# Optimization experiments

Hardware: AMD Instinct MI355X
Metric: run time of the kernel (lower is better)

Reference implementation:

```python
import jax, jax.numpy as jnp
import numpy as np
import math

B, S, D, H, F, L = 16, 512, 1024, 16, 4096, 4
DK = D // H
NEG = -1e32


def _cosine_pe(max_len, d_model):
    # deterministic sin/cos table (the 0.1*randn init is fully overwritten for even d_model)
    pos = np.arange(max_len, dtype=np.float32)[:, None]
    div = np.exp(np.arange(0, d_model, 2, dtype=np.float32) * (-(math.log(10000.0) / d_model)))
    pe = np.zeros((max_len, d_model), dtype=np.float32)
    pe[:, 0::2] = np.sin(pos * div)
    pe[:, 1::2] = np.cos(pos * div)
    return jnp.asarray(pe)[None]  # [1, max_len, D]


def setup_inputs() -> dict:
    key = jax.random.key(0)
    ks = jax.random.split(key, 16)
    sc_d = 1.0 / math.sqrt(D)
    sc_f = 1.0 / math.sqrt(F)
    return {
        "q_embed_data": jax.random.normal(ks[0], (B, S, D), jnp.float32),
        "qa_embed_data": jax.random.normal(ks[1], (B, S, D), jnp.float32),
        "pe": _cosine_pe(S, D),
        "Wk": jax.random.normal(ks[2], (L, D, D), jnp.float32) * sc_d,
        "bk": jnp.zeros((L, D), jnp.float32),
        "Wv": jax.random.normal(ks[3], (L, D, D), jnp.float32) * sc_d,
        "bv": jnp.zeros((L, D), jnp.float32),
        "Wo": jax.random.normal(ks[4], (L, D, D), jnp.float32) * sc_d,
        "bo": jnp.zeros((L, D), jnp.float32),
        "ln1_g": jnp.ones((L, D), jnp.float32),
        "ln1_b": jnp.zeros((L, D), jnp.float32),
        "W1": jax.random.normal(ks[5], (L, D, F), jnp.float32) * sc_d,
        "b1": jnp.zeros((L, F), jnp.float32),
        "W2": jax.random.normal(ks[6], (L, F, D), jnp.float32) * sc_f,
        "b2": jnp.zeros((L, D), jnp.float32),
        "ln2_g": jnp.ones((L, D), jnp.float32),
        "ln2_b": jnp.zeros((L, D), jnp.float32),
    }


def _layer_norm(x, g, b, eps=1e-5):
    mu = jnp.mean(x, axis=-1, keepdims=True)
    var = jnp.var(x, axis=-1, keepdims=True)
    return (x - mu) * jax.lax.rsqrt(var + eps) * g + b


def _forward(q_embed_data, qa_embed_data, pe, Wk, bk, Wv, bv, Wo, bo,
             ln1_g, ln1_b, W1, b1, W2, b2, ln2_g, ln2_b):
    x = q_embed_data + pe[:, :S, :]
    y = qa_embed_data + pe[:, :S, :]  # values stay fixed across blocks
    # mask=0 in TransformerLayer: triu(k=0)==0 -> strictly-lower-triangular allowed
    allowed = jnp.tril(jnp.ones((S, S), bool), k=-1)  # [S, S]
    row_keep = (jnp.arange(S) > 0).astype(x.dtype)[None, None, :, None]  # zero_pad row 0
    scale = 1.0 / math.sqrt(DK)
    for l in range(L):
        # kq_same: q and k both use k_linear
        qk = (x @ Wk[l] + bk[l]).reshape(B, S, H, DK).transpose(0, 2, 1, 3)  # [B,H,S,DK]
        v = (y @ Wv[l] + bv[l]).reshape(B, S, H, DK).transpose(0, 2, 1, 3)
        scores = jnp.einsum('bhqd,bhkd->bhqk', qk, qk) * scale
        scores = jnp.where(allowed, scores, NEG)
        attn = jax.nn.softmax(scores, axis=-1) * row_keep  # zero_pad: first query row -> zeros
        ctx = jnp.einsum('bhqk,bhkd->bhqd', attn, v)
        ctx = ctx.transpose(0, 2, 1, 3).reshape(B, S, D)
        x = _layer_norm(x + (ctx @ Wo[l] + bo[l]), ln1_g[l], ln1_b[l])
        ffn = jax.nn.relu(x @ W1[l] + b1[l]) @ W2[l] + b2[l]
        x = _layer_norm(x + ffn, ln2_g[l], ln2_b[l])
    return x


def reference(q_embed_data, qa_embed_data, pe, Wk, bk, Wv, bv, Wo, bo,
              ln1_g, ln1_b, W1, b1, W2, b2, ln2_g, ln2_b):
    return _forward(q_embed_data, qa_embed_data, pe, Wk, bk, Wv, bv, Wo, bo,
                    ln1_g, ln1_b, W1, b1, W2, b2, ln2_g, ln2_b)
```

## Files before the change

kernel.cpp:

```cpp
#include <hip/hip_runtime.h>
#include <stdint.h>

typedef unsigned short u16;
typedef __bf16 bf16x8 __attribute__((ext_vector_type(8)));
typedef float f32x4 __attribute__((ext_vector_type(4)));

#define BDIM 16
#define SLEN 512
#define DMODEL 1024
#define NHEAD 16
#define DHEAD 64
#define FDIM 4096
#define NLAYER 4
#define ROWS (BDIM*SLEN)
#define KVT 64

__device__ __forceinline__ u16 f2b(float f) {
  uint32_t u = __builtin_bit_cast(uint32_t, f);
  u = (u + 0x7fffu + ((u >> 16) & 1u)) >> 16;
  return (u16)u;
}
__device__ __forceinline__ float b2f_lo(uint32_t u) {
  return __builtin_bit_cast(float, u << 16);
}
__device__ __forceinline__ float b2f_hi(uint32_t u) {
  return __builtin_bit_cast(float, u & 0xffff0000u);
}

__device__ __forceinline__ void gl_lds16(const void* g, void* l) {
  uint32_t loff = (uint32_t)(uintptr_t)l;
  __builtin_amdgcn_global_load_lds(
      (__attribute__((address_space(1))) uint32_t*)(uintptr_t)g,
      (__attribute__((address_space(3))) uint32_t*)loff,
      16, 0, 0);
}

__global__ __launch_bounds__(256) void prep_kernel(const float4* __restrict__ q,
                                                   const float4* __restrict__ qa,
                                                   const float4* __restrict__ pe,
                                                   float4* __restrict__ x,
                                                   u16* __restrict__ xb,
                                                   u16* __restrict__ yb) {
  int idx = blockIdx.x * 256 + threadIdx.x;
  int pidx = idx & (SLEN * DMODEL / 4 - 1);
  float4 qv = q[idx], av = qa[idx], pv = pe[pidx];
  float4 xv = make_float4(qv.x + pv.x, qv.y + pv.y, qv.z + pv.z, qv.w + pv.w);
  float4 yv = make_float4(av.x + pv.x, av.y + pv.y, av.z + pv.z, av.w + pv.w);
  x[idx] = xv;
  uint32_t x0 = (uint32_t)f2b(xv.x) | ((uint32_t)f2b(xv.y) << 16);
  uint32_t x1 = (uint32_t)f2b(xv.z) | ((uint32_t)f2b(xv.w) << 16);
  uint32_t y0 = (uint32_t)f2b(yv.x) | ((uint32_t)f2b(yv.y) << 16);
  uint32_t y1 = (uint32_t)f2b(yv.z) | ((uint32_t)f2b(yv.w) << 16);
  ((uint2*)xb)[idx] = make_uint2(x0, x1);
  ((uint2*)yb)[idx] = make_uint2(y0, y1);
}

__global__ __launch_bounds__(256) void transpose_f2b(const float* __restrict__ in,
                                                     u16* __restrict__ out,
                                                     int M, int N) {
  __shared__ float t[32][33];
  int tx = threadIdx.x & 31, ty = threadIdx.x >> 5;
  int m0 = blockIdx.y * 32, n0 = blockIdx.x * 32;
  #pragma unroll
  for (int i = 0; i < 32; i += 8) t[ty + i][tx] = in[(size_t)(m0 + ty + i) * N + n0 + tx];
  __syncthreads();
  #pragma unroll
  for (int i = 0; i < 32; i += 8) out[(size_t)(n0 + ty + i) * M + m0 + tx] = f2b(t[tx][ty + i]);
}

template<int BN, bool RELU, bool BF16OUT>
__global__ __launch_bounds__(512, 2) void gemm8p(const u16* __restrict__ Ap,
                                                 const u16* __restrict__ Bp,
                                                 const float* __restrict__ bias,
                                                 void* __restrict__ Cp,
                                                 int M, int N, int K) {
  constexpr int NBH = BN / 128;
  constexpr int NREP = BN / 64;
  constexpr int QN = NREP / 2;
  constexpr int HU = 8192;
  __shared__ __attribute__((aligned(16))) u16 lds[2][(2 + NBH) * HU];

  const int tid = threadIdx.x, wave = tid >> 6, lane = tid & 63;
  const int lg = lane >> 4, lc = lane & 15;
  const int wm = wave >> 2, wn = wave & 3;

  const int gx = gridDim.x;
  int nwg = gx * gridDim.y;
  int orig = blockIdx.y * gx + blockIdx.x;
  int qq = nwg >> 3, rr_ = nwg & 7;
  int xcd = orig & 7, ix = orig >> 3;
  int wg = (xcd < rr_ ? xcd * (qq + 1) : rr_ * (qq + 1) + (xcd - rr_) * qq) + ix;
  const int m0 = (wg / gx) * 256, n0 = (wg % gx) * BN;

  const int ldbyte = K * 2;
  const char* Ag = (const char*)Ap + (size_t)m0 * ldbyte;
  const char* Bg = (const char*)Bp + (size_t)n0 * ldbyte;

  int o1 = tid * 16, o2 = 8192 + tid * 16;
  int sr1 = o1 >> 7, sg1 = (((o1 >> 4) & 7) - sr1) & 7;
  int sr2 = o2 >> 7, sg2 = (((o2 >> 4) & 7) - sr2) & 7;
  const int soff1 = sr1 * ldbyte + sg1 * 16;
  const int soff2 = sr2 * ldbyte + sg2 * 16;
  const int NT = K >> 6;

  auto stageA = [&](int kt, int h, int buf) {
    const char* g = Ag + (size_t)h * 128 * ldbyte + (size_t)kt * 128;
    char* d = (char*)&lds[buf][h * HU] + wave * 1024;
    gl_lds16(g + soff1, d);
    gl_lds16(g + soff2, d + 8192);
  };
  auto stageB = [&](int kt, int h, int buf) {
    const char* g = Bg + (size_t)h * 128 * ldbyte + (size_t)kt * 128;
    char* d = (char*)&lds[buf][(2 + h) * HU] + wave * 1024;
    gl_lds16(g + soff1, d);
    gl_lds16(g + soff2, d + 8192);
  };

  const int bstart = wn * (BN / 4);
  const int bh = bstart >> 7, bc0 = bstart & 127;

  auto rdA = [&](const u16* base, int f, int kk) -> bf16x8 {
    int row = f * 16 + lc;
    return *(const bf16x8*)&base[row * 64 + (((kk * 4 + lg + row) & 7) << 3)];
  };
  auto rdB = [&](const u16* base, int jj, int kk) -> bf16x8 {
    int row = bc0 + jj * 16 + lc;
    return *(const bf16x8*)&base[row * 64 + (((kk * 4 + lg + row) & 7) << 3)];
  };

  f32x4 acc[8][NREP];
  #pragma unroll
  for (int f = 0; f < 8; f++)
    #pragma unroll
    for (int j = 0; j < NREP; j++) acc[f][j] = (f32x4){0.f, 0.f, 0.f, 0.f};

  stageA(0, 0, 0); stageA(0, 1, 0);
  stageB(0, 0, 0); if (NBH == 2) stageB(0, 1, 0);
  stageA(1, 0, 1); stageA(1, 1, 1);
  asm volatile("s_waitcnt vmcnt(4)\n\ts_barrier" ::: "memory");

  auto ktile = [&](int k, int buf) {
    const u16* Ab_ = &lds[buf][wm * HU];
    const u16* Bb_ = &lds[buf][(2 + bh) * HU];
    const int kn = (k + 1 < NT) ? k + 1 : NT - 1;
    const int k2 = (k + 2 < NT) ? k + 2 : NT - 1;
    bf16x8 a0[4][2], a1[4][2], b0[QN][2], b1[QN][2];

    #pragma unroll
    for (int f = 0; f < 4; f++) { a0[f][0] = rdA(Ab_, f, 0); a0[f][1] = rdA(Ab_, f, 1); }
    #pragma unroll
    for (int j = 0; j < QN; j++) { b0[j][0] = rdB(Bb_, j, 0); b0[j][1] = rdB(Bb_, j, 1); }
    stageB(kn, 0, buf ^ 1);
    asm volatile("s_barrier" ::: "memory");
    __builtin_amdgcn_s_setprio(1);
    #pragma unroll
    for (int f = 0; f < 4; f++)
      #pragma unroll
      for (int j = 0; j < QN; j++) {
        acc[f][j] = __builtin_amdgcn_mfma_f32_16x16x32_bf16(a0[f][0], b0[j][0], acc[f][j], 0, 0, 0);
        acc[f][j] = __builtin_amdgcn_mfma_f32_16x16x32_bf16(a0[f][1], b0[j][1], acc[f][j], 0, 0, 0);
      }
    __builtin_amdgcn_s_setprio(0);
    asm volatile("s_barrier" ::: "memory");

    #pragma unroll
    for (int f = 0; f < 4; f++) { a1[f][0] = rdA(Ab_, 4 + f, 0); a1[f][1] = rdA(Ab_, 4 + f, 1); }
    if (NBH == 2) stageB(kn, 1, buf ^ 1);
    asm volatile("s_barrier" ::: "memory");
    __builtin_amdgcn_s_setprio(1);
    #pragma unroll
    for (int f = 0; f < 4; f++)
      #pragma unroll
      for (int j = 0; j < QN; j++) {
        acc[4 + f][j] = __builtin_amdgcn_mfma_f32_16x16x32_bf16(a1[f][0], b0[j][0], acc[4 + f][j], 0, 0, 0);
        acc[4 + f][j] = __builtin_amdgcn_mfma_f32_16x16x32_bf16(a1[f][1], b0[j][1], acc[4 + f][j], 0, 0, 0);
      }
    __builtin_amdgcn_s_setprio(0);
    asm volatile("s_barrier" ::: "memory");

    #pragma unroll
    for (int j = 0; j < QN; j++) { b1[j][0] = rdB(Bb_, QN + j, 0); b1[j][1] = rdB(Bb_, QN + j, 1); }
    stageA(k2, 0, buf);
    asm volatile("s_barrier" ::: "memory");
    __builtin_amdgcn_s_setprio(1);
    #pragma unroll
    for (int f = 0; f < 4; f++)
      #pragma unroll
      for (int j = 0; j < QN; j++) {
        acc[4 + f][QN + j] = __builtin_amdgcn_mfma_f32_16x16x32_bf16(a1[f][0], b1[j][0], acc[4 + f][QN + j], 0, 0, 0);
        acc[4 + f][QN + j] = __builtin_amdgcn_mfma_f32_16x16x32_bf16(a1[f][1], b1[j][1], acc[4 + f][QN + j], 0, 0, 0);
      }
    __builtin_amdgcn_s_setprio(0);
    asm volatile("s_barrier" ::: "memory");

    stageA(k2, 1, buf);
    asm volatile("s_barrier" ::: "memory");
    __builtin_amdgcn_s_setprio(1);
    #pragma unroll
    for (int f = 0; f < 4; f++)
      #pragma unroll
      for (int j = 0; j < QN; j++) {
        acc[f][QN + j] = __builtin_amdgcn_mfma_f32_16x16x32_bf16(a0[f][0], b1[j][0], acc[f][QN + j], 0, 0, 0);
        acc[f][QN + j] = __builtin_amdgcn_mfma_f32_16x16x32_bf16(a0[f][1], b1[j][1], acc[f][QN + j], 0, 0, 0);
      }
    __builtin_amdgcn_s_setprio(0);
    asm volatile("s_waitcnt vmcnt(4)\n\ts_barrier" ::: "memory");
  };

  for (int k = 0; k < NT; k += 2) {
    ktile(k, 0);
    ktile(k + 1, 1);
  }

  #pragma unroll
  for (int f = 0; f < 8; f++) {
    int row = m0 + wm * 128 + f * 16 + lg * 4;
    #pragma unroll
    for (int j = 0; j < NREP; j++) {
      int col = n0 + bstart + j * 16 + lc;
      float bv = bias[col];
      #pragma unroll
      for (int t2 = 0; t2 < 4; t2++) {
        float v = acc[f][j][t2] + bv;
        if (RELU) v = fmaxf(v, 0.f);
        if (BF16OUT) ((u16*)Cp)[(size_t)(row + t2) * N + col] = f2b(v);
        else         ((float*)Cp)[(size_t)(row + t2) * N + col] = v;
      }
    }
  }
}

__global__ __launch_bounds__(256, 4) void attn_kernel(const u16* __restrict__ QK,
                                                      const u16* __restrict__ V,
                                                      u16* __restrict__ CTX) {
  __shared__ __attribute__((aligned(16))) u16 Ks[2][KVT * 64];
  __shared__ __attribute__((aligned(16))) u16 VTs[64 * 72];
  __shared__ __attribute__((aligned(16))) u16 Ps[4][16 * 72];
  const int qt = blockIdx.x, bh = blockIdx.y;
  const int b = bh >> 4, h = bh & 15;
  const char* Qg = (const char*)(QK + (size_t)b * SLEN * DMODEL + h * DHEAD);
  const char* Vg = (const char*)(V + (size_t)b * SLEN * DMODEL + h * DHEAD);
  const int tid = threadIdx.x, wave = tid >> 6, lane = tid & 63;
  const int lg = lane >> 4, lc = lane & 15;
  const int ktmax = qt;

  auto stageK = [&](int kt, int buf) {
    #pragma unroll
    for (int i = 0; i < 2; i++) {
      int o = i * 4096 + tid * 16;
      int row = o >> 7, slot = (o >> 4) & 7;
      int g = (slot - row) & 7;
      gl_lds16(Qg + (size_t)(kt * KVT + row) * (DMODEL * 2) + g * 16,
               (char*)Ks[buf] + i * 4096 + wave * 1024);
    }
  };
  const int vhi = lane >> 5, vls = lane & 31;
  const int vc_ = wave + 4 * vhi;
  auto loadV = [&](int kt, uint4 (&va)[2]) {
    const char* src = Vg + (size_t)(kt * KVT + 2 * vls) * (DMODEL * 2) + vc_ * 16;
    va[0] = *(const uint4*)src;
    va[1] = *(const uint4*)(src + DMODEL * 2);
  };
  auto writeVT = [&](const uint4 (&va)[2]) {
    u16 e0[8], e1[8];
    *(uint4*)e0 = va[0];
    *(uint4*)e1 = va[1];
    #pragma unroll
    for (int j = 0; j < 8; j++) {
      uint32_t pk = (uint32_t)e0[j] | ((uint32_t)e1[j] << 16);
      *(uint32_t*)&VTs[(8 * vc_ + j) * 72 + 2 * vls] = pk;
    }
  };

  uint4 vaA[2], vaB[2];
  const int qrow = qt * 64 + wave * 16 + lc;
  bf16x8 aq0 = *(const bf16x8*)(Qg + (size_t)qrow * (DMODEL * 2) + lg * 16);
  bf16x8 aq1 = *(const bf16x8*)(Qg + (size_t)qrow * (DMODEL * 2) + 64 + lg * 16);
  stageK(0, 0);
  loadV(0, vaA);
  stageK(ktmax > 0 ? 1 : 0, 1);
  asm volatile("s_waitcnt vmcnt(2)\n\ts_barrier" ::: "memory");

  float l_run[4] = {0.f, 0.f, 0.f, 0.f};
  f32x4 acc_o[4];
  #pragma unroll
  for (int n = 0; n < 4; n++) acc_o[n] = (f32x4){0.f, 0.f, 0.f, 0.f};

  auto iter = [&](int kt, int cur, uint4 (&vc)[2], uint4 (&vn)[2]) {
    const int kn = (kt + 1 <= ktmax) ? kt + 1 : ktmax;
    const int k2 = (kt + 2 <= ktmax) ? kt + 2 : ktmax;

    asm volatile("s_waitcnt vmcnt(2)" ::: "memory");
    __builtin_amdgcn_s_barrier();
    writeVT(vc);
    loadV(kn, vn);

    f32x4 sc[4];
    #pragma unroll
    for (int n = 0; n < 4; n++) sc[n] = (f32x4){0.f, 0.f, 0.f, 0.f};
    #pragma unroll
    for (int n = 0; n < 4; n++) {
      int row = n * 16 + lc;
      bf16x8 bk0 = *(const bf16x8*)&Ks[cur][row * 64 + (((lg + row) & 7) << 3)];
      bf16x8 bk1 = *(const bf16x8*)&Ks[cur][row * 64 + (((4 + lg + row) & 7) << 3)];
      sc[n] = __builtin_amdgcn_mfma_f32_16x16x32_bf16(aq0, bk0, sc[n], 0, 0, 0);
      sc[n] = __builtin_amdgcn_mfma_f32_16x16x32_bf16(aq1, bk1, sc[n], 0, 0, 0);
    }

    const int qbase = qt * 64 + wave * 16 + lg * 4;
    #pragma unroll
    for (int n = 0; n < 4; n++) {
      int kg = kt * KVT + n * 16 + lc;
      #pragma unroll
      for (int r = 0; r < 4; r++) {
        float e = __expf(fmaf(sc[n][r], 0.125f, -24.f));
        float p = (kg < qbase + r) ? e : 0.f;
        l_run[r] += p;
        Ps[wave][(lg * 4 + r) * 72 + n * 16 + lc] = f2b(p);
      }
    }

    asm volatile("s_waitcnt lgkmcnt(0)" ::: "memory");
    __builtin_amdgcn_s_barrier();
    stageK(k2, cur);

    bf16x8 ap0 = *(const bf16x8*)&Ps[wave][lc * 72 + lg * 8];
    bf16x8 ap1 = *(const bf16x8*)&Ps[wave][lc * 72 + 32 + lg * 8];
    #pragma unroll
    for (int n2 = 0; n2 < 4; n2++) {
      bf16x8 bv0 = *(const bf16x8*)&VTs[(n2 * 16 + lc) * 72 + lg * 8];
      bf16x8 bv1 = *(const bf16x8*)&VTs[(n2 * 16 + lc) * 72 + 32 + lg * 8];
      acc_o[n2] = __builtin_amdgcn_mfma_f32_16x16x32_bf16(ap0, bv0, acc_o[n2], 0, 0, 0);
      acc_o[n2] = __builtin_amdgcn_mfma_f32_16x16x32_bf16(ap1, bv1, acc_o[n2], 0, 0, 0);
    }
  };

  for (int kt = 0; kt <= ktmax; kt += 2) {
    iter(kt, 0, vaA, vaB);
    if (kt + 1 <= ktmax) iter(kt + 1, 1, vaB, vaA);
  }

  #pragma unroll
  for (int d = 1; d < 16; d <<= 1)
    #pragma unroll
    for (int r = 0; r < 4; r++) l_run[r] += __shfl_xor(l_run[r], d, 64);

  asm volatile("s_waitcnt vmcnt(0)" ::: "memory");
  #pragma unroll
  for (int n2 = 0; n2 < 4; n2++)
    #pragma unroll
    for (int r = 0; r < 4; r++) {
      int sq = qt * 64 + wave * 16 + lg * 4 + r;
      float v = (sq == 0) ? 0.f : acc_o[n2][r] / l_run[r];
      CTX[((size_t)b * SLEN + sq) * DMODEL + h * DHEAD + n2 * 16 + lc] = f2b(v);
    }
}

__global__ __launch_bounds__(256) void ln_kernel(const u16* __restrict__ tmp,
                                                 float* __restrict__ x,
                                                 u16* __restrict__ xb,
                                                 const float* __restrict__ gw,
                                                 const float* __restrict__ bw) {
  __shared__ float red[4], red2[4];
  const int row = blockIdx.x, t = threadIdx.x;
  const size_t base = (size_t)row * DMODEL + t * 4;
  float4 xv = *(const float4*)&x[base];
  uint2 tv = *(const uint2*)&tmp[base];
  float v[4];
  v[0] = xv.x + b2f_lo(tv.x); v[1] = xv.y + b2f_hi(tv.x);
  v[2] = xv.z + b2f_lo(tv.y); v[3] = xv.w + b2f_hi(tv.y);
  float s = v[0] + v[1] + v[2] + v[3];
  #pragma unroll
  for (int d = 1; d < 64; d <<= 1) s += __shfl_xor(s, d, 64);
  if ((t & 63) == 0) red[t >> 6] = s;
  __syncthreads();
  float mean = (red[0] + red[1] + red[2] + red[3]) * (1.f / DMODEL);
  float q2 = 0.f;
  #pragma unroll
  for (int i = 0; i < 4; i++) { float d_ = v[i] - mean; q2 += d_ * d_; }
  #pragma unroll
  for (int d = 1; d < 64; d <<= 1) q2 += __shfl_xor(q2, d, 64);
  if ((t & 63) == 0) red2[t >> 6] = q2;
  __syncthreads();
  float var = (red2[0] + red2[1] + red2[2] + red2[3]) * (1.f / DMODEL);
  float rs = rsqrtf(var + 1e-5f);
  float4 gv = *(const float4*)&gw[t * 4];
  float4 bv4 = *(const float4*)&bw[t * 4];
  float o0 = (v[0] - mean) * rs * gv.x + bv4.x;
  float o1 = (v[1] - mean) * rs * gv.y + bv4.y;
  float o2 = (v[2] - mean) * rs * gv.z + bv4.z;
  float o3 = (v[3] - mean) * rs * gv.w + bv4.w;
  *(float4*)&x[base] = make_float4(o0, o1, o2, o3);
  uint2 pk;
  pk.x = (uint32_t)f2b(o0) | ((uint32_t)f2b(o1) << 16);
  pk.y = (uint32_t)f2b(o2) | ((uint32_t)f2b(o3) << 16);
  *(uint2*)&xb[base] = pk;
}

__global__ __launch_bounds__(256) void copy_f4(const float4* __restrict__ src, float4* __restrict__ dst) {
  int i = blockIdx.x * 256 + threadIdx.x;
  dst[i] = src[i];
}

extern "C" void kernel_launch(void* const* d_in, const int* in_sizes, int n_in,
                              void* d_out, int out_size, void* d_ws, size_t ws_size,
                              hipStream_t stream) {
  (void)in_sizes; (void)n_in; (void)out_size; (void)ws_size;
  const float* q    = (const float*)d_in[0];
  const float* qa   = (const float*)d_in[1];
  const float* pe   = (const float*)d_in[2];
  const float* Wk   = (const float*)d_in[3];
  const float* bk   = (const float*)d_in[4];
  const float* Wv   = (const float*)d_in[5];
  const float* bv   = (const float*)d_in[6];
  const float* Wo   = (const float*)d_in[7];
  const float* bo   = (const float*)d_in[8];
  const float* ln1g = (const float*)d_in[9];
  const float* ln1b = (const float*)d_in[10];
  const float* W1   = (const float*)d_in[11];
  const float* b1   = (const float*)d_in[12];
  const float* W2   = (const float*)d_in[13];
  const float* b2   = (const float*)d_in[14];
  const float* ln2g = (const float*)d_in[15];
  const float* ln2b = (const float*)d_in[16];

  char* w = (char*)d_ws;
  float* x_f32 = (float*)w; w += (size_t)ROWS * DMODEL * 4;
  u16* xb   = (u16*)w; w += (size_t)ROWS * DMODEL * 2;
  u16* yb   = (u16*)w; w += (size_t)ROWS * DMODEL * 2;
  u16* qkb  = (u16*)w; w += (size_t)ROWS * DMODEL * 2;
  u16* vb   = (u16*)w; w += (size_t)ROWS * DMODEL * 2;
  u16* ctxb = (u16*)w; w += (size_t)ROWS * DMODEL * 2;
  u16* ffnb = (u16*)w; w += (size_t)ROWS * FDIM * 2;
  u16* WkT  = (u16*)w; w += (size_t)DMODEL * DMODEL * 2;
  u16* WvT  = (u16*)w; w += (size_t)DMODEL * DMODEL * 2;
  u16* WoT  = (u16*)w; w += (size_t)DMODEL * DMODEL * 2;
  u16* W1T  = (u16*)w; w += (size_t)DMODEL * FDIM * 2;
  u16* W2T  = (u16*)w; w += (size_t)DMODEL * FDIM * 2;
  u16* tmpb = qkb;

  prep_kernel<<<ROWS * DMODEL / 4 / 256, 256, 0, stream>>>(
      (const float4*)q, (const float4*)qa, (const float4*)pe, (float4*)x_f32, xb, yb);

  for (int l = 0; l < NLAYER; l++) {
    transpose_f2b<<<dim3(32, 32), 256, 0, stream>>>(Wk + (size_t)l * DMODEL * DMODEL, WkT, DMODEL, DMODEL);
    transpose_f2b<<<dim3(32, 32), 256, 0, stream>>>(Wv + (size_t)l * DMODEL * DMODEL, WvT, DMODEL, DMODEL);
    transpose_f2b<<<dim3(32, 32), 256, 0, stream>>>(Wo + (size_t)l * DMODEL * DMODEL, WoT, DMODEL, DMODEL);
    transpose_f2b<<<dim3(128, 32), 256, 0, stream>>>(W1 + (size_t)l * DMODEL * FDIM, W1T, DMODEL, FDIM);
    transpose_f2b<<<dim3(32, 128), 256, 0, stream>>>(W2 + (size_t)l * FDIM * DMODEL, W2T, FDIM, DMODEL);

    gemm8p<128, false, true><<<dim3(DMODEL / 128, ROWS / 256), 512, 0, stream>>>(
        xb, WkT, bk + l * DMODEL, qkb, ROWS, DMODEL, DMODEL);
    gemm8p<128, false, true><<<dim3(DMODEL / 128, ROWS / 256), 512, 0, stream>>>(
        yb, WvT, bv + l * DMODEL, vb, ROWS, DMODEL, DMODEL);
    attn_kernel<<<dim3(SLEN / 64, BDIM * NHEAD), 256, 0, stream>>>(qkb, vb, ctxb);
    gemm8p<128, false, true><<<dim3(DMODEL / 128, ROWS / 256), 512, 0, stream>>>(
        ctxb, WoT, bo + l * DMODEL, tmpb, ROWS, DMODEL, DMODEL);
    ln_kernel<<<ROWS, 256, 0, stream>>>(tmpb, x_f32, xb, ln1g + l * DMODEL, ln1b + l * DMODEL);
    gemm8p<256, true, true><<<dim3(FDIM / 256, ROWS / 256), 512, 0, stream>>>(
        xb, W1T, b1 + l * FDIM, ffnb, ROWS, FDIM, DMODEL);
    gemm8p<128, false, true><<<dim3(DMODEL / 128, ROWS / 256), 512, 0, stream>>>(
        ffnb, W2T, b2 + l * DMODEL, tmpb, ROWS, DMODEL, FDIM);
    ln_kernel<<<ROWS, 256, 0, stream>>>(tmpb, x_f32, xb, ln2g + l * DMODEL, ln2b + l * DMODEL);
  }
  copy_f4<<<ROWS * DMODEL / 4 / 256, 256, 0, stream>>>((const float4*)x_f32, (float4*)d_out);
}
```

Measured before the change: 1.237 ms.

## Add 128x128 four-wave GEMM kernel for N=1024 projections

Adds a new bf16 MFMA GEMM kernel with 128x128 tiles, four waves, XCD-aware block remapping, swizzled LDS, double-buffered async global-to-LDS staging, and setprio around MFMA bursts. It replaces the 256x128 eight-wave gemm8p for the K, V, O and W2 projections, doubling the number of workgroups from 256 to 512. The aim is better CU occupancy and load balance on the many-CU device for these N=1024 GEMMs. The cost is less data reuse per tile, so global and LDS traffic per FLOP goes up.

```diff
diff --git a/kernel.cpp b/kernel.cpp
--- a/kernel.cpp
+++ b/kernel.cpp
@@ -226,6 +226,102 @@
         if (BF16OUT) ((u16*)Cp)[(size_t)(row + t2) * N + col] = f2b(v);
         else         ((float*)Cp)[(size_t)(row + t2) * N + col] = v;
       }
+    }
+  }
+}
+
+__global__ __launch_bounds__(256, 2) void gemm4w(const u16* __restrict__ Ap,
+                                                 const u16* __restrict__ Bp,
+                                                 const float* __restrict__ bias,
+                                                 u16* __restrict__ Cp,
+                                                 int M, int N, int K) {
+  __shared__ __attribute__((aligned(16))) u16 As[2][128 * 64];
+  __shared__ __attribute__((aligned(16))) u16 Bs[2][128 * 64];
+  const int tid = threadIdx.x, wave = tid >> 6, lane = tid & 63;
+  const int lg = lane >> 4, lc = lane & 15;
+  const int wm = wave >> 1, wn = wave & 1;
+
+  const int gx = gridDim.x;
+  int nwg = gx * gridDim.y;
+  int orig = blockIdx.y * gx + blockIdx.x;
+  int qq = nwg >> 3, rr_ = nwg & 7;
+  int xcd = orig & 7, ix = orig >> 3;
+  int wg = (xcd < rr_ ? xcd * (qq + 1) : rr_ * (qq + 1) + (xcd - rr_) * qq) + ix;
+  const int m0 = (wg / gx) * 128, n0 = (wg % gx) * 128;
+
+  const int ldbyte = K * 2;
+  const char* Ag = (const char*)Ap + (size_t)m0 * ldbyte;
+  const char* Bg = (const char*)Bp + (size_t)n0 * ldbyte;
+  const int NT = K >> 6;
+
+  auto stage = [&](const char* gb, int kt, u16* lb) {
+    #pragma unroll
+    for (int c = 0; c < 4; c++) {
+      int o = c * 4096 + tid * 16;
+      int row = o >> 7;
+      int g = (((o >> 4) & 7) - row) & 7;
+      gl_lds16(gb + (size_t)row * ldbyte + (size_t)kt * 128 + g * 16,
+               (char*)lb + c * 4096 + wave * 1024);
+    }
+  };
+  auto rd = [&](const u16* base, int strip, int f, int kk) -> bf16x8 {
+    int row = strip * 64 + f * 16 + lc;
+    return *(const bf16x8*)&base[row * 64 + (((kk * 4 + lg + row) & 7) << 3)];
+  };
+
+  f32x4 acc[4][4];
+  #pragma unroll
+  for (int f = 0; f < 4; f++)
+    #pragma unroll
+    for (int n = 0; n < 4; n++) acc[f][n] = (f32x4){0.f, 0.f, 0.f, 0.f};
+
+  stage(Ag, 0, As[0]); stage(Bg, 0, Bs[0]);
+  stage(Ag, 1, As[1]); stage(Bg, 1, Bs[1]);
+  asm volatile("s_waitcnt vmcnt(8)\n\ts_barrier" ::: "memory");
+
+  for (int k = 0; k < NT; k++) {
+    const int buf = k & 1;
+    const int k2 = (k + 2 < NT) ? k + 2 : NT - 1;
+    bf16x8 a[4][2], b[4][2];
+    #pragma unroll
+    for (int f = 0; f < 4; f++) { a[f][0] = rd(As[buf], wm, f, 0); a[f][1] = rd(As[buf], wm, f, 1); }
+    #pragma unroll
+    for (int n = 0; n < 4; n++) { b[n][0] = rd(Bs[buf], wn, n, 0); b[n][1] = rd(Bs[buf], wn, n, 1); }
+    asm volatile("s_barrier" ::: "memory");
+    __builtin_amdgcn_s_setprio(1);
+    #pragma unroll
+    for (int f = 0; f < 4; f++)
+      #pragma unroll
+      for (int n = 0; n < 2; n++) {
+        acc[f][n] = __builtin_amdgcn_mfma_f32_16x16x32_bf16(a[f][0], b[n][0], acc[f][n], 0, 0, 0);
+        acc[f][n] = __builtin_amdgcn_mfma_f32_16x16x32_bf16(a[f][1], b[n][1], acc[f][n], 0, 0, 0);
+      }
+    __builtin_amdgcn_s_setprio(0);
+    asm volatile("s_barrier" ::: "memory");
+    stage(Ag, k2, As[buf]);
+    stage(Bg, k2, Bs[buf]);
+    __builtin_amdgcn_s_setprio(1);
+    #pragma unroll
+    for (int f = 0; f < 4; f++)
+      #pragma unroll
+      for (int n = 2; n < 4; n++) {
+        acc[f][n] = __builtin_amdgcn_mfma_f32_16x16x32_bf16(a[f][0], b[n][0], acc[f][n], 0, 0, 0);
+        acc[f][n] = __builtin_amdgcn_mfma_f32_16x16x32_bf16(a[f][1], b[n][1], acc[f][n], 0, 0, 0);
+      }
+    __builtin_amdgcn_s_setprio(0);
+    asm volatile("s_waitcnt vmcnt(8)\n\ts_barrier" ::: "memory");
+  }
+
+  #pragma unroll
+  for (int f = 0; f < 4; f++) {
+    int row = m0 + wm * 64 + f * 16 + lg * 4;
+    #pragma unroll
+    for (int n = 0; n < 4; n++) {
+      int col = n0 + wn * 64 + n * 16 + lc;
+      float bv = bias[col];
+      #pragma unroll
+      for (int r = 0; r < 4; r++)
+        Cp[(size_t)(row + r) * N + col] = f2b(acc[f][n][r] + bv);
     }
   }
 }
@@ -449,17 +545,17 @@
     transpose_f2b<<<dim3(128, 32), 256, 0, stream>>>(W1 + (size_t)l * DMODEL * FDIM, W1T, DMODEL, FDIM);
     transpose_f2b<<<dim3(32, 128), 256, 0, stream>>>(W2 + (size_t)l * FDIM * DMODEL, W2T, FDIM, DMODEL);
 
-    gemm8p<128, false, true><<<dim3(DMODEL / 128, ROWS / 256), 512, 0, stream>>>(
+    gemm4w<<<dim3(DMODEL / 128, ROWS / 128), 256, 0, stream>>>(
         xb, WkT, bk + l * DMODEL, qkb, ROWS, DMODEL, DMODEL);
-    gemm8p<128, false, true><<<dim3(DMODEL / 128, ROWS / 256), 512, 0, stream>>>(
+    gemm4w<<<dim3(DMODEL / 128, ROWS / 128), 256, 0, stream>>>(
         yb, WvT, bv + l * DMODEL, vb, ROWS, DMODEL, DMODEL);
     attn_kernel<<<dim3(SLEN / 64, BDIM * NHEAD), 256, 0, stream>>>(qkb, vb, ctxb);
-    gemm8p<128, false, true><<<dim3(DMODEL / 128, ROWS / 256), 512, 0, stream>>>(
+    gemm4w<<<dim3(DMODEL / 128, ROWS / 128), 256, 0, stream>>>(
         ctxb, WoT, bo + l * DMODEL, tmpb, ROWS, DMODEL, DMODEL);
     ln_kernel<<<ROWS, 256, 0, stream>>>(tmpb, x_f32, xb, ln1g + l * DMODEL, ln1b + l * DMODEL);
     gemm8p<256, true, true><<<dim3(FDIM / 256, ROWS / 256), 512, 0, stream>>>(
         xb, W1T, b1 + l * FDIM, ffnb, ROWS, FDIM, DMODEL);
-    gemm8p<128, false, true><<<dim3(DMODEL / 128, ROWS / 256), 512, 0, stream>>>(
+    gemm4w<<<dim3(DMODEL / 128, ROWS / 128), 256, 0, stream>>>(
         ffnb, W2T, b2 + l * DMODEL, tmpb, ROWS, DMODEL, FDIM);
     ln_kernel<<<ROWS, 256, 0, stream>>>(tmpb, x_f32, xb, ln2g + l * DMODEL, ln2b + l * DMODEL);
   }
```

After: 1.188 ms. -3.9%, faster.
